# Kernel tuning notes

Measured on AMD Instinct MI355X. Metric: run time of the kernel, lower is better.

## Reference

```python
import jax, jax.numpy as jnp
import numpy as np

N_NODES = 100000
E = 1600000
IN_C = 128
OUT_C = 128


def setup_inputs() -> dict:
    key = jax.random.key(0)
    k1, k2, k3, k4, k5, k6 = jax.random.split(key, 6)
    x = jax.random.normal(k1, (N_NODES, IN_C), dtype=jnp.float32)
    edge_index = jax.random.randint(k2, (2, E), 0, N_NODES, dtype=jnp.int64)
    s = 1.0 / np.sqrt(IN_C)
    W_src = jax.random.uniform(k3, (OUT_C, IN_C), minval=-s, maxval=s, dtype=jnp.float32)
    b_src = jax.random.uniform(k4, (OUT_C,), minval=-s, maxval=s, dtype=jnp.float32)
    W_dst = jax.random.uniform(k5, (OUT_C, IN_C), minval=-s, maxval=s, dtype=jnp.float32)
    b_dst = jax.random.uniform(k6, (OUT_C,), minval=-s, maxval=s, dtype=jnp.float32)
    return {"x": x, "edge_index": edge_index, "W_src": W_src, "b_src": b_src,
            "W_dst": W_dst, "b_dst": b_dst}


def reference(x, edge_index, W_src, b_src, W_dst, b_dst):
    src, dst = edge_index[0], edge_index[1]
    x_j = x[src]                                             # [E, in]
    agg_sum = jax.ops.segment_sum(x_j, dst, num_segments=x.shape[0])   # [N, in]
    cnt = jax.ops.segment_sum(jnp.ones((src.shape[0],), dtype=x.dtype), dst,
                              num_segments=x.shape[0])       # [N]
    agg_mean = agg_sum / jnp.maximum(cnt, 1.0)[:, None]      # scatter-mean (empty -> 0)
    return agg_mean @ W_src.T + b_src + x @ W_dst.T + b_dst
```

## Files before the change

kernel.cpp:

```cpp
#include <hip/hip_runtime.h>
#include <stdint.h>

typedef __attribute__((ext_vector_type(8))) short short8;
typedef __attribute__((ext_vector_type(4))) float floatx4;
typedef __attribute__((ext_vector_type(4))) int intx4;
typedef __attribute__((ext_vector_type(2))) int intx2;
typedef __attribute__((ext_vector_type(2))) float floatx2;

#define NN 100000
#define NE 1600000
#define NB_SCAN 196
#define HIST_BLKS 6250
#define CONV_BLKS 6250
#define NODES_PER_G 12500
#define CAP 64

#define NBKT 196
#define TILE 4096
#define BIN_BLKS 391
#define CAPB 8704

__device__ __forceinline__ short f2bf(float f) {
  unsigned u = __builtin_bit_cast(unsigned, f);
  u = (u + 0x7fffu + ((u >> 16) & 1u)) >> 16;
  return (short)u;
}
__device__ __forceinline__ float bf2f(unsigned hi16) {
  return __builtin_bit_cast(float, hi16 << 16);
}

#define BK_GC_B 0
#define BK_GBUF_B 4096
#define BK_SLOT_B 14000000
#define BK_ROW_B 21000000
#define BK_DEG_B 21500000
#define BK_XB_B 22000000
#define BK_XQ_B 47600000
#define BK_NEED 60400000ull

#define WS_DEG 0
#define WS_ROW 100000
#define WS_CUR 200000
#define WS_BSUM 300000
#define WS_BOFF 300256
#define WS_SLOT 300512
#define WS_XB_BYTE 7602048


__global__ __launch_bounds__(256) void bin_conv_k(const int* __restrict__ ei,
                                                  int* __restrict__ gcount,
                                                  int2* __restrict__ gbuf,
                                                  const float* __restrict__ x,
                                                  short* __restrict__ xb,
                                                  int* __restrict__ xq) {
  const int blk = blockIdx.x;
  if (blk < BIN_BLKS) {
    __shared__ int ls[TILE], ld[TILE];
    __shared__ int hcnt[NBKT], hbase[NBKT], hcur[NBKT], gposs[NBKT];
    __shared__ int sc[256];
    __shared__ int ntot;
    const int tid = threadIdx.x;
    const int tile = blk * TILE;

    int s_[16], d_[16];
#pragma unroll
    for (int k = 0; k < 16; ++k) {
      const int e = tile + tid + k * 256;
      if (e < NE) {
        s_[k] = ei[e];
        d_[k] = ei[NE + e];
      } else {
        s_[k] = 0; d_[k] = -1;
      }
    }
    if (tid < NBKT) hcnt[tid] = 0;
    __syncthreads();
#pragma unroll
    for (int k = 0; k < 16; ++k)
      if (d_[k] >= 0) atomicAdd(&hcnt[d_[k] >> 9], 1);
    __syncthreads();
    sc[tid] = (tid < NBKT) ? hcnt[tid] : 0;
    __syncthreads();
    for (int off = 1; off < 256; off <<= 1) {
      const int v = (tid >= off) ? sc[tid - off] : 0;
      __syncthreads();
      sc[tid] += v;
      __syncthreads();
    }
    if (tid < NBKT) {
      hbase[tid] = sc[tid] - hcnt[tid];
      gposs[tid] = atomicAdd(&gcount[tid], hcnt[tid]);
      hcur[tid] = 0;
    }
    if (tid == 0) ntot = sc[NBKT - 1];
    __syncthreads();
#pragma unroll
    for (int k = 0; k < 16; ++k) {
      if (d_[k] >= 0) {
        const int b = d_[k] >> 9;
        const int r = hbase[b] + atomicAdd(&hcur[b], 1);
        ls[r] = s_[k];
        ld[r] = d_[k];
      }
    }
    __syncthreads();
    const int nt = ntot;
    for (int i = tid; i < nt; i += 256) {
      const int d = ld[i];
      const int b = d >> 9;
      const int pos = gposs[b] + (i - hbase[b]);
      if (pos < CAPB) {
        int2 e; e.x = ls[i]; e.y = d;
        gbuf[(size_t)b * CAPB + pos] = e;
      }
    }
  } else {
    const int t = (blk - BIN_BLKS) * 256 + threadIdx.x;
    const floatx4* x4 = reinterpret_cast<const floatx4*>(x);
    floatx4 f0 = __builtin_nontemporal_load(&x4[2 * t]);
    floatx4 f1 = __builtin_nontemporal_load(&x4[2 * t + 1]);
    short8 v;
    v[0] = f2bf(f0.x); v[1] = f2bf(f0.y); v[2] = f2bf(f0.z); v[3] = f2bf(f0.w);
    v[4] = f2bf(f1.x); v[5] = f2bf(f1.y); v[6] = f2bf(f1.z); v[7] = f2bf(f1.w);
    reinterpret_cast<short8*>(xb)[t] = v;
    int w0 = __builtin_amdgcn_cvt_pk_fp8_f32(f0.x, f0.y, 0, false);
    w0 = __builtin_amdgcn_cvt_pk_fp8_f32(f0.z, f0.w, w0, true);
    int w1 = __builtin_amdgcn_cvt_pk_fp8_f32(f1.x, f1.y, 0, false);
    w1 = __builtin_amdgcn_cvt_pk_fp8_f32(f1.z, f1.w, w1, true);
    intx2 q; q.x = w0; q.y = w1;
    reinterpret_cast<intx2*>(xq)[t] = q;
  }
}

__global__ __launch_bounds__(512) void bucket_csr_k(const int* __restrict__ gcount,
                                                    const int2* __restrict__ gbuf,
                                                    int* __restrict__ slotg,
                                                    int* __restrict__ rowstg,
                                                    int* __restrict__ degg) {
  __shared__ int cnt[512], sc[512], cur[512];
  __shared__ int lslot[CAPB];
  const int b = blockIdx.x;
  const int tid = threadIdx.x;
  const int nb = min(gcount[b], CAPB);
  const size_t base = (size_t)b * CAPB;

  cnt[tid] = 0;
  __syncthreads();
  for (int i = tid; i < nb; i += 512)
    atomicAdd(&cnt[gbuf[base + i].y & 511], 1);
  __syncthreads();
  sc[tid] = cnt[tid];
  __syncthreads();
  for (int off = 1; off < 512; off <<= 1) {
    const int v = (tid >= off) ? sc[tid - off] : 0;
    __syncthreads();
    sc[tid] += v;
    __syncthreads();
  }
  const int rst = sc[tid] - cnt[tid];
  cur[tid] = rst;
  __syncthreads();
  for (int i = tid; i < nb; i += 512) {
    const int2 e = gbuf[base + i];
    const int p = atomicAdd(&cur[e.y & 511], 1);
    lslot[p] = e.x << 6;
  }
  __syncthreads();
  for (int i = tid; i < nb; i += 512) slotg[base + i] = lslot[i];
  const int n = b * 512 + tid;
  if (n < NN) {
    rowstg[n] = (int)base + rst;
    degg[n] = cnt[tid];
  }
}

__global__ __launch_bounds__(256) void gather_csr_k(const unsigned short* __restrict__ xq,
                                                    const int* __restrict__ rowstg,
                                                    const int* __restrict__ degg,
                                                    const int* __restrict__ slotg,
                                                    float* __restrict__ out) {
  const int lane = threadIdx.x & 63;
  const int w = (blockIdx.x * 256 + threadIdx.x) >> 6;
  if (w >= NN) return;
  const int st = rowstg[w];
  const int dg = degg[w];
  float2 acc = {0.f, 0.f};
  for (int b0 = 0; b0 < dg; b0 += 64) {
    const int nbk = min(64, dg - b0);
    const int idx = (lane < nbk) ? slotg[st + b0 + lane] : 0;
    int i = 0;
    for (; i + 4 <= nbk; i += 4) {
      const int s0 = __shfl(idx, i), s1 = __shfl(idx, i + 1);
      const int s2 = __shfl(idx, i + 2), s3 = __shfl(idx, i + 3);
      const int v0 = xq[s0 + lane];
      const int v1 = xq[s1 + lane];
      const int v2 = xq[s2 + lane];
      const int v3 = xq[s3 + lane];
      floatx2 p0 = __builtin_amdgcn_cvt_pk_f32_fp8(v0, false);
      floatx2 p1 = __builtin_amdgcn_cvt_pk_f32_fp8(v1, false);
      floatx2 p2 = __builtin_amdgcn_cvt_pk_f32_fp8(v2, false);
      floatx2 p3 = __builtin_amdgcn_cvt_pk_f32_fp8(v3, false);
      acc.x += p0.x; acc.y += p0.y;
      acc.x += p1.x; acc.y += p1.y;
      acc.x += p2.x; acc.y += p2.y;
      acc.x += p3.x; acc.y += p3.y;
    }
    for (; i < nbk; ++i) {
      const int s = __shfl(idx, i);
      const int v = xq[s + lane];
      floatx2 p = __builtin_amdgcn_cvt_pk_f32_fp8(v, false);
      acc.x += p.x; acc.y += p.y;
    }
  }
  const float inv = 1.0f / fmaxf((float)dg, 1.0f);
  float2 r = {acc.x * inv, acc.y * inv};
  reinterpret_cast<float2*>(out)[(size_t)w * 64 + lane] = r;
}


__global__ __launch_bounds__(256) void hist_conv_k(const int* __restrict__ ei,
                                                   int* __restrict__ deg,
                                                   const float* __restrict__ x,
                                                   short* __restrict__ xb) {
  const int b = blockIdx.x;
  if (b < HIST_BLKS) {
    int e = b * 256 + threadIdx.x;
    if (e < NE) atomicAdd(&deg[ei[NE + e]], 1);
  } else {
    const int t = (b - HIST_BLKS) * 256 + threadIdx.x;
    const float4* x4 = reinterpret_cast<const float4*>(x);
    float4 f0 = x4[2 * t];
    float4 f1 = x4[2 * t + 1];
    short8 v;
    v[0] = f2bf(f0.x); v[1] = f2bf(f0.y); v[2] = f2bf(f0.z); v[3] = f2bf(f0.w);
    v[4] = f2bf(f1.x); v[5] = f2bf(f1.y); v[6] = f2bf(f1.z); v[7] = f2bf(f1.w);
    reinterpret_cast<short8*>(xb)[t] = v;
  }
}

__global__ __launch_bounds__(256) void scan1_k(const int* __restrict__ deg,
                                               int* __restrict__ bsum) {
  __shared__ int s[256];
  const int t = threadIdx.x;
  const int i0 = blockIdx.x * 512 + 2 * t;
  int v = 0;
  if (i0 < NN) v += deg[i0];
  if (i0 + 1 < NN) v += deg[i0 + 1];
  s[t] = v;
  __syncthreads();
  for (int off = 128; off > 0; off >>= 1) {
    if (t < off) s[t] += s[t + off];
    __syncthreads();
  }
  if (t == 0) bsum[blockIdx.x] = s[0];
}

__global__ __launch_bounds__(256) void scan2_k(const int* __restrict__ bsum,
                                               int* __restrict__ boff) {
  __shared__ int s[256];
  const int t = threadIdx.x;
  const int v = (t < NB_SCAN) ? bsum[t] : 0;
  s[t] = v;
  __syncthreads();
  for (int off = 1; off < 256; off <<= 1) {
    int a = (t >= off) ? s[t - off] : 0;
    __syncthreads();
    s[t] += a;
    __syncthreads();
  }
  if (t < NB_SCAN) boff[t] = s[t] - v;
}

__global__ __launch_bounds__(256) void scan3_k(const int* __restrict__ deg,
                                               const int* __restrict__ boff,
                                               int* __restrict__ rowst,
                                               int* __restrict__ cursor) {
  __shared__ int s[256];
  const int t = threadIdx.x;
  const int i0 = blockIdx.x * 512 + 2 * t;
  const int v0 = (i0 < NN) ? deg[i0] : 0;
  const int v1 = (i0 + 1 < NN) ? deg[i0 + 1] : 0;
  const int tsum = v0 + v1;
  s[t] = tsum;
  __syncthreads();
  for (int off = 1; off < 256; off <<= 1) {
    int a = (t >= off) ? s[t - off] : 0;
    __syncthreads();
    s[t] += a;
    __syncthreads();
  }
  const int excl = s[t] - tsum + boff[blockIdx.x];
  if (i0 < NN) { rowst[i0] = excl; cursor[i0] = excl; }
  if (i0 + 1 < NN) { rowst[i0 + 1] = excl + v0; cursor[i0 + 1] = excl + v0; }
}

__global__ __launch_bounds__(256) void fill_k(const int* __restrict__ ei,
                                              int* __restrict__ cursor,
                                              int* __restrict__ slot) {
  const int g = blockIdx.x & 7;
  const int lo = g * NODES_PER_G;
  const int hi = lo + NODES_PER_G;
  const int stride = (gridDim.x >> 3) * 256;
  for (int e = (blockIdx.x >> 3) * 256 + threadIdx.x; e < NE; e += stride) {
    const int d = ei[NE + e];
    if (d >= lo && d < hi) {
      const int p = atomicAdd(&cursor[d], 1);
      slot[p] = ei[e];
    }
  }
}

__global__ __launch_bounds__(256) void gather_bf_k(const short* __restrict__ xb,
                                                   const int* __restrict__ rowst,
                                                   const int* __restrict__ deg,
                                                   const int* __restrict__ slot,
                                                   float* __restrict__ out) {
  const int lane = threadIdx.x & 63;
  const int w = (blockIdx.x * 256 + threadIdx.x) >> 6;
  if (w >= NN) return;
  const int st = rowst[w];
  const int dg = deg[w];
  const unsigned* xu = reinterpret_cast<const unsigned*>(xb);
  float2 acc = {0.f, 0.f};
  for (int b0 = 0; b0 < dg; b0 += 64) {
    const int nb = min(64, dg - b0);
    const int idx = (lane < nb) ? slot[st + b0 + lane] : 0;
    for (int i = 0; i < nb; ++i) {
      const int s = __shfl(idx, i);
      unsigned u = xu[(size_t)s * 64 + lane];
      acc.x += bf2f(u & 0xffffu); acc.y += bf2f(u >> 16);
    }
  }
  const float inv = 1.0f / fmaxf((float)dg, 1.0f);
  float2 r = {acc.x * inv, acc.y * inv};
  reinterpret_cast<float2*>(out)[(size_t)w * 64 + lane] = r;
}

__global__ __launch_bounds__(512) void sage_gemm_k(
    const float* __restrict__ mean, const short* __restrict__ xb,
    const float* __restrict__ Wsrc, const float* __restrict__ bsrc,
    const float* __restrict__ Wdst, const float* __restrict__ bdst,
    float* __restrict__ out) {
  __shared__ short Alds[128 * 256];
  __shared__ short Blds[128 * 256];
  const int tid = threadIdx.x;
  const int n0 = blockIdx.x * 128;

  {
    const int j = tid >> 2;
    const int q = tid & 3;
    const float* src = (q < 2) ? (Wsrc + j * 128 + q * 64)
                               : (Wdst + j * 128 + (q - 2) * 64);
    const int sw = (j & 7) << 4;
    const int base = j * 512 + q * 128;
#pragma unroll
    for (int c = 0; c < 8; ++c) {
      float4 f0 = reinterpret_cast<const float4*>(src)[2 * c];
      float4 f1 = reinterpret_cast<const float4*>(src)[2 * c + 1];
      short8 v;
      v[0] = f2bf(f0.x); v[1] = f2bf(f0.y); v[2] = f2bf(f0.z); v[3] = f2bf(f0.w);
      v[4] = f2bf(f1.x); v[5] = f2bf(f1.y); v[6] = f2bf(f1.z); v[7] = f2bf(f1.w);
      *reinterpret_cast<short8*>(reinterpret_cast<char*>(Blds) + ((base + c * 16) ^ sw)) = v;
    }
  }
  {
    const int r = tid >> 2;
    const int q = tid & 3;
    const int n = n0 + r;
    const int sw = (r & 7) << 4;
    const int base = r * 512 + q * 128;
    if (n < NN) {
      if (q >= 2) {
        const short8* src8 = reinterpret_cast<const short8*>(
            xb + (size_t)n * 128 + (q - 2) * 64);
#pragma unroll
        for (int c = 0; c < 8; ++c)
          *reinterpret_cast<short8*>(reinterpret_cast<char*>(Alds) + ((base + c * 16) ^ sw)) = src8[c];
      } else {
        const float* src = mean + (size_t)n * 128 + q * 64;
#pragma unroll
        for (int c = 0; c < 8; ++c) {
          float4 f0 = reinterpret_cast<const float4*>(src)[2 * c];
          float4 f1 = reinterpret_cast<const float4*>(src)[2 * c + 1];
          short8 v;
          v[0] = f2bf(f0.x); v[1] = f2bf(f0.y); v[2] = f2bf(f0.z); v[3] = f2bf(f0.w);
          v[4] = f2bf(f1.x); v[5] = f2bf(f1.y); v[6] = f2bf(f1.z); v[7] = f2bf(f1.w);
          *reinterpret_cast<short8*>(reinterpret_cast<char*>(Alds) + ((base + c * 16) ^ sw)) = v;
        }
      }
    } else {
      short8 z = {};
#pragma unroll
      for (int c = 0; c < 8; ++c)
        *reinterpret_cast<short8*>(reinterpret_cast<char*>(Alds) + ((base + c * 16) ^ sw)) = z;
    }
  }
  __syncthreads();

  const int wid = tid >> 6;
  const int lane = tid & 63;
  const int r0 = wid * 16;
  const int lrow = lane & 15;
  const int kh = (lane >> 4) * 8;
  const int arow = r0 + lrow;
  const int asw = (arow & 7) << 4;

  floatx4 acc[8];
  floatx4 zero = {0.f, 0.f, 0.f, 0.f};
#pragma unroll
  for (int f = 0; f < 8; ++f) acc[f] = zero;

#pragma unroll
  for (int ks = 0; ks < 8; ++ks) {
    const int kb = (ks * 32 + kh) * 2;
    short8 a = *reinterpret_cast<const short8*>(
        reinterpret_cast<const char*>(Alds) + ((arow * 512 + kb) ^ asw));
#pragma unroll
    for (int f = 0; f < 8; ++f) {
      const int j = f * 16 + lrow;
      short8 b = *reinterpret_cast<const short8*>(
          reinterpret_cast<const char*>(Blds) + ((j * 512 + kb) ^ ((j & 7) << 4)));
      acc[f] = __builtin_amdgcn_mfma_f32_16x16x32_bf16(a, b, acc[f], 0, 0, 0);
    }
  }

  const int crow = r0 + (lane >> 4) * 4;
#pragma unroll
  for (int f = 0; f < 8; ++f) {
    const int j = f * 16 + lrow;
    const float bias = bsrc[j] + bdst[j];
#pragma unroll
    for (int rg = 0; rg < 4; ++rg) {
      const int n = n0 + crow + rg;
      if (n < NN) out[(size_t)n * 128 + j] = acc[f][rg] + bias;
    }
  }
}

extern "C" void kernel_launch(void* const* d_in, const int* in_sizes, int n_in,
                              void* d_out, int out_size, void* d_ws, size_t ws_size,
                              hipStream_t stream) {
  const float* x = (const float*)d_in[0];
  const int* ei = (const int*)d_in[1];
  const float* Wsrc = (const float*)d_in[2];
  const float* bsrc = (const float*)d_in[3];
  const float* Wdst = (const float*)d_in[4];
  const float* bdst = (const float*)d_in[5];
  float* out = (float*)d_out;

  if (ws_size >= BK_NEED) {
    int* gcount = (int*)((char*)d_ws + BK_GC_B);
    int2* gbuf = (int2*)((char*)d_ws + BK_GBUF_B);
    int* slotg = (int*)((char*)d_ws + BK_SLOT_B);
    int* rowstg = (int*)((char*)d_ws + BK_ROW_B);
    int* degg = (int*)((char*)d_ws + BK_DEG_B);
    short* xb = (short*)((char*)d_ws + BK_XB_B);
    int* xq = (int*)((char*)d_ws + BK_XQ_B);
    hipMemsetAsync(gcount, 0, NBKT * sizeof(int), stream);
    bin_conv_k<<<BIN_BLKS + CONV_BLKS, 256, 0, stream>>>(ei, gcount, gbuf, x, xb, xq);
    bucket_csr_k<<<NBKT, 512, 0, stream>>>(gcount, gbuf, slotg, rowstg, degg);
    gather_csr_k<<<(NN * 64 + 255) / 256, 256, 0, stream>>>(
        (const unsigned short*)xq, rowstg, degg, slotg, out);
    sage_gemm_k<<<(NN + 127) / 128, 512, 0, stream>>>(out, xb, Wsrc, bsrc,
                                                      Wdst, bdst, out);
    return;
  }

  int* ws = (int*)d_ws;
  int* deg = ws + WS_DEG;
  int* rowst = ws + WS_ROW;
  int* cursor = ws + WS_CUR;
  int* bsum = ws + WS_BSUM;
  int* boff = ws + WS_BOFF;
  int* slot = ws + WS_SLOT;
  short* xb = (short*)((char*)d_ws + WS_XB_BYTE);

  hipMemsetAsync(deg, 0, NN * sizeof(int), stream);
  hist_conv_k<<<HIST_BLKS + CONV_BLKS, 256, 0, stream>>>(ei, deg, x, xb);
  scan1_k<<<NB_SCAN, 256, 0, stream>>>(deg, bsum);
  scan2_k<<<1, 256, 0, stream>>>(bsum, boff);
  scan3_k<<<NB_SCAN, 256, 0, stream>>>(deg, boff, rowst, cursor);
  fill_k<<<1024, 256, 0, stream>>>(ei, cursor, slot);
  gather_bf_k<<<(NN * 64 + 255) / 256, 256, 0, stream>>>(xb, rowst, deg, slot, out);
  sage_gemm_k<<<(NN + 127) / 128, 512, 0, stream>>>(out, xb, Wsrc, bsrc, Wdst, bdst, out);
}
```

Baseline: 148.8 us.

## Store aggregated mean as bf16 in output buffer and split GEMM K-loop

The gather kernels now round the per-node mean to bf16 and pack it into the upper half of each output row, instead of writing a full fp32 row. The GEMM reads that packed bf16 data directly, so it no longer converts the mean from fp32. This halves the mean's write and read traffic through the intermediate. The GEMM also stages the K dimension in two halves, first the mean with W_src and then x with W_dst, which halves its LDS footprint to allow more resident blocks, at the cost of an extra pair of barriers. Correctness depends on each GEMM block reading its own rows' packed mean before overwriting those same rows with the fp32 result.

```diff
diff --git a/kernel.cpp b/kernel.cpp
--- a/kernel.cpp
+++ b/kernel.cpp
@@ -213,8 +213,9 @@
     }
   }
   const float inv = 1.0f / fmaxf((float)dg, 1.0f);
-  float2 r = {acc.x * inv, acc.y * inv};
-  reinterpret_cast<float2*>(out)[(size_t)w * 64 + lane] = r;
+  const unsigned b0w = (unsigned)(unsigned short)f2bf(acc.x * inv);
+  const unsigned b1w = (unsigned)(unsigned short)f2bf(acc.y * inv);
+  reinterpret_cast<unsigned*>(out + (size_t)w * 128 + 64)[lane] = b0w | (b1w << 16);
 }
 
 
@@ -332,70 +333,20 @@
     }
   }
   const float inv = 1.0f / fmaxf((float)dg, 1.0f);
-  float2 r = {acc.x * inv, acc.y * inv};
-  reinterpret_cast<float2*>(out)[(size_t)w * 64 + lane] = r;
+  const unsigned b0w = (unsigned)(unsigned short)f2bf(acc.x * inv);
+  const unsigned b1w = (unsigned)(unsigned short)f2bf(acc.y * inv);
+  reinterpret_cast<unsigned*>(out + (size_t)w * 128 + 64)[lane] = b0w | (b1w << 16);
 }
 
 __global__ __launch_bounds__(512) void sage_gemm_k(
-    const float* __restrict__ mean, const short* __restrict__ xb,
+    const short* __restrict__ xb,
     const float* __restrict__ Wsrc, const float* __restrict__ bsrc,
     const float* __restrict__ Wdst, const float* __restrict__ bdst,
     float* __restrict__ out) {
-  __shared__ short Alds[128 * 256];
-  __shared__ short Blds[128 * 256];
+  __shared__ short Alds[128 * 128];
+  __shared__ short Blds[128 * 128];
   const int tid = threadIdx.x;
   const int n0 = blockIdx.x * 128;
-
-  {
-    const int j = tid >> 2;
-    const int q = tid & 3;
-    const float* src = (q < 2) ? (Wsrc + j * 128 + q * 64)
-                               : (Wdst + j * 128 + (q - 2) * 64);
-    const int sw = (j & 7) << 4;
-    const int base = j * 512 + q * 128;
-#pragma unroll
-    for (int c = 0; c < 8; ++c) {
-      float4 f0 = reinterpret_cast<const float4*>(src)[2 * c];
-      float4 f1 = reinterpret_cast<const float4*>(src)[2 * c + 1];
-      short8 v;
-      v[0] = f2bf(f0.x); v[1] = f2bf(f0.y); v[2] = f2bf(f0.z); v[3] = f2bf(f0.w);
-      v[4] = f2bf(f1.x); v[5] = f2bf(f1.y); v[6] = f2bf(f1.z); v[7] = f2bf(f1.w);
-      *reinterpret_cast<short8*>(reinterpret_cast<char*>(Blds) + ((base + c * 16) ^ sw)) = v;
-    }
-  }
-  {
-    const int r = tid >> 2;
-    const int q = tid & 3;
-    const int n = n0 + r;
-    const int sw = (r & 7) << 4;
-    const int base = r * 512 + q * 128;
-    if (n < NN) {
-      if (q >= 2) {
-        const short8* src8 = reinterpret_cast<const short8*>(
-            xb + (size_t)n * 128 + (q - 2) * 64);
-#pragma unroll
-        for (int c = 0; c < 8; ++c)
-          *reinterpret_cast<short8*>(reinterpret_cast<char*>(Alds) + ((base + c * 16) ^ sw)) = src8[c];
-      } else {
-        const float* src = mean + (size_t)n * 128 + q * 64;
-#pragma unroll
-        for (int c = 0; c < 8; ++c) {
-          float4 f0 = reinterpret_cast<const float4*>(src)[2 * c];
-          float4 f1 = reinterpret_cast<const float4*>(src)[2 * c + 1];
-          short8 v;
-          v[0] = f2bf(f0.x); v[1] = f2bf(f0.y); v[2] = f2bf(f0.z); v[3] = f2bf(f0.w);
-          v[4] = f2bf(f1.x); v[5] = f2bf(f1.y); v[6] = f2bf(f1.z); v[7] = f2bf(f1.w);
-          *reinterpret_cast<short8*>(reinterpret_cast<char*>(Alds) + ((base + c * 16) ^ sw)) = v;
-        }
-      }
-    } else {
-      short8 z = {};
-#pragma unroll
-      for (int c = 0; c < 8; ++c)
-        *reinterpret_cast<short8*>(reinterpret_cast<char*>(Alds) + ((base + c * 16) ^ sw)) = z;
-    }
-  }
-  __syncthreads();
 
   const int wid = tid >> 6;
   const int lane = tid & 63;
@@ -411,17 +362,61 @@
   for (int f = 0; f < 8; ++f) acc[f] = zero;
 
 #pragma unroll
-  for (int ks = 0; ks < 8; ++ks) {
-    const int kb = (ks * 32 + kh) * 2;
-    short8 a = *reinterpret_cast<const short8*>(
-        reinterpret_cast<const char*>(Alds) + ((arow * 512 + kb) ^ asw));
-#pragma unroll
-    for (int f = 0; f < 8; ++f) {
-      const int j = f * 16 + lrow;
-      short8 b = *reinterpret_cast<const short8*>(
-          reinterpret_cast<const char*>(Blds) + ((j * 512 + kb) ^ ((j & 7) << 4)));
-      acc[f] = __builtin_amdgcn_mfma_f32_16x16x32_bf16(a, b, acc[f], 0, 0, 0);
-    }
+  for (int h = 0; h < 2; ++h) {
+    {
+      const int j = tid >> 2;
+      const int q = tid & 3;
+      const float* src = ((h == 0) ? Wsrc : Wdst) + j * 128 + q * 32;
+      const int sw = (j & 7) << 4;
+      const int base = j * 256 + q * 64;
+#pragma unroll
+      for (int c = 0; c < 4; ++c) {
+        float4 f0 = reinterpret_cast<const float4*>(src)[2 * c];
+        float4 f1 = reinterpret_cast<const float4*>(src)[2 * c + 1];
+        short8 v;
+        v[0] = f2bf(f0.x); v[1] = f2bf(f0.y); v[2] = f2bf(f0.z); v[3] = f2bf(f0.w);
+        v[4] = f2bf(f1.x); v[5] = f2bf(f1.y); v[6] = f2bf(f1.z); v[7] = f2bf(f1.w);
+        *reinterpret_cast<short8*>(reinterpret_cast<char*>(Blds) + ((base + c * 16) ^ sw)) = v;
+      }
+    }
+    {
+      const int r = tid >> 2;
+      const int q = tid & 3;
+      const int n = n0 + r;
+      const int sw = (r & 7) << 4;
+      const int base = r * 256 + q * 64;
+      if (n < NN) {
+        const char* srcb = (h == 0)
+            ? (reinterpret_cast<const char*>(out + (size_t)n * 128 + 64) + q * 64)
+            : (reinterpret_cast<const char*>(xb + (size_t)n * 128) + q * 64);
+#pragma unroll
+        for (int c = 0; c < 4; ++c) {
+          short8 v = *reinterpret_cast<const short8*>(srcb + c * 16);
+          *reinterpret_cast<short8*>(reinterpret_cast<char*>(Alds) + ((base + c * 16) ^ sw)) = v;
+        }
+      } else {
+        short8 z = {};
+#pragma unroll
+        for (int c = 0; c < 4; ++c)
+          *reinterpret_cast<short8*>(reinterpret_cast<char*>(Alds) + ((base + c * 16) ^ sw)) = z;
+      }
+    }
+    __syncthreads();
+
+#pragma unroll
+    for (int ks = 0; ks < 4; ++ks) {
+      const int kb = (ks * 32 + kh) * 2;
+      short8 a = *reinterpret_cast<const short8*>(
+          reinterpret_cast<const char*>(Alds) + ((arow * 256 + kb) ^ asw));
+#pragma unroll
+      for (int f = 0; f < 8; ++f) {
+        const int j = f * 16 + lrow;
+        short8 b = *reinterpret_cast<const short8*>(
+            reinterpret_cast<const char*>(Blds) + ((j * 256 + kb) ^ ((j & 7) << 4)));
+        acc[f] = __builtin_amdgcn_mfma_f32_16x16x32_bf16(a, b, acc[f], 0, 0, 0);
+      }
+    }
+    __syncthreads();
   }
 
   const int crow = r0 + (lane >> 4) * 4;
@@ -461,7 +456,7 @@
     bucket_csr_k<<<NBKT, 512, 0, stream>>>(gcount, gbuf, slotg, rowstg, degg);
     gather_csr_k<<<(NN * 64 + 255) / 256, 256, 0, stream>>>(
         (const unsigned short*)xq, rowstg, degg, slotg, out);
-    sage_gemm_k<<<(NN + 127) / 128, 512, 0, stream>>>(out, xb, Wsrc, bsrc,
+    sage_gemm_k<<<(NN + 127) / 128, 512, 0, stream>>>(xb, Wsrc, bsrc,
                                                       Wdst, bdst, out);
     return;
   }
@@ -482,5 +477,5 @@
   scan3_k<<<NB_SCAN, 256, 0, stream>>>(deg, boff, rowst, cursor);
   fill_k<<<1024, 256, 0, stream>>>(ei, cursor, slot);
   gather_bf_k<<<(NN * 64 + 255) / 256, 256, 0, stream>>>(xb, rowst, deg, slot, out);
-  sage_gemm_k<<<(NN + 127) / 128, 512, 0, stream>>>(out, xb, Wsrc, bsrc, Wdst, bdst, out);
-}
+  sage_gemm_k<<<(NN + 127) / 128, 512, 0, stream>>>(xb, Wsrc, bsrc, Wdst, bdst, out);
+}
```

Result: faster. 143.4 us (-3.6%).
